# Kernel optimization log

Hardware: AMD Instinct MI355X
Metric: run time of the kernel (lower is better)

## Reference

```python
import jax, jax.numpy as jnp
import numpy as np

N = 50000          # nodes
E = 800000         # edges (avg degree 16)
# (in_feats, out_feats, num_heads) per GATConv layer
LAYERS = [(128, 64, 4), (256, 64, 2), (128, 64, 2), (128, 64, 1), (64, 4, 1)]
NEG_SLOPE = 0.2    # DGL GATConv default


def setup_inputs() -> dict:
    key = jax.random.key(0)
    ks = jax.random.split(key, 3 + 4 * len(LAYERS))
    inp = {
        "x": jax.random.normal(ks[0], (N, 128), jnp.float32),
        "src": jax.random.randint(ks[1], (E,), 0, N, jnp.int32),
        "dst": jax.random.randint(ks[2], (E,), 0, N, jnp.int32),
    }
    for i, (fin, fout, h) in enumerate(LAYERS, start=1):
        k = 3 + 4 * (i - 1)
        inp[f"W{i}"] = (jax.random.normal(ks[k], (fin, h * fout), jnp.float32)
                        / np.float32(np.sqrt(fin)))
        inp[f"al{i}"] = jax.random.normal(ks[k + 1], (h, fout), jnp.float32) * 0.1
        inp[f"ar{i}"] = jax.random.normal(ks[k + 2], (h, fout), jnp.float32) * 0.1
        inp[f"b{i}"] = jnp.zeros((h * fout,), jnp.float32)
    return inp


def gat_layer(x, src, dst, W, al, ar, b):
    """DGL GATConv: linear -> per-edge LeakyReLU scores -> edge softmax by dst -> weighted sum + bias."""
    H, F = al.shape
    n = x.shape[0]
    z = (x @ W).reshape(n, H, F)                      # [N,H,F]
    el = jnp.einsum('nhf,hf->nh', z, al)              # src-side score
    er = jnp.einsum('nhf,hf->nh', z, ar)              # dst-side score
    e = jax.nn.leaky_relu(el[src] + er[dst], NEG_SLOPE)   # [E,H]
    # segment softmax over incoming edges of each dst node
    m = jax.ops.segment_max(e, dst, num_segments=n)   # -inf for empty segments (unused)
    ex = jnp.exp(e - m[dst])
    s = jax.ops.segment_sum(ex, dst, num_segments=n)
    alpha = ex / s[dst]                               # [E,H]
    out = jax.ops.segment_sum(alpha[:, :, None] * z[src], dst, num_segments=n)  # [N,H,F]
    return out + b.reshape(1, H, F)


def reference(x, src, dst,
              W1, al1, ar1, b1,
              W2, al2, ar2, b2,
              W3, al3, ar3, b3,
              W4, al4, ar4, b4,
              W5, al5, ar5, b5):
    h = gat_layer(x, src, dst, W1, al1, ar1, b1)
    h = jax.nn.elu(h).reshape(h.shape[0], -1)
    h = gat_layer(h, src, dst, W2, al2, ar2, b2)
    h = jax.nn.elu(h).reshape(h.shape[0], -1)
    h = gat_layer(h, src, dst, W3, al3, ar3, b3)
    h = jax.nn.elu(h).reshape(h.shape[0], -1)
    h = gat_layer(h, src, dst, W4, al4, ar4, b4)
    h = jax.nn.elu(h).reshape(h.shape[0], -1)
    h = gat_layer(h, src, dst, W5, al5, ar5, b5)
    return h.reshape(h.shape[0], -1)
```

## Files before the change

kernel.cpp:

```cpp
#include <hip/hip_runtime.h>
#include <hip/hip_bf16.h>

#define NN 50000
#define NE 800000

typedef __attribute__((ext_vector_type(8))) short s16x8;
typedef __attribute__((ext_vector_type(4))) float f32x4;

__device__ __forceinline__ float bf2f(unsigned short u) {
  union { unsigned int i; float f; } v; v.i = ((unsigned int)u) << 16; return v.f;
}
__device__ __forceinline__ unsigned short f2bf(float f) {
  union { unsigned int i; float f; } v; v.f = f;
  unsigned int x = v.i;
  return (unsigned short)((x + 0x7FFFu + ((x >> 16) & 1u)) >> 16);
}

__global__ void k_detect(const unsigned short* __restrict__ xh, int* __restrict__ flag) {
  int t = threadIdx.x;
  float b0 = bf2f(xh[2 * t]);
  float b1 = bf2f(xh[2 * t + 1]);
  bool ok = (b0 == b0) && (b1 == b1) && fabsf(b0) < 64.f && fabsf(b1) < 64.f;
  unsigned long long m = __ballot(ok);
  if (t == 0) *flag = (m == ~0ull) ? 1 : 0;
}

__global__ void k_cvt_x(const void* __restrict__ src, unsigned short* __restrict__ dst, int n,
                        const int* __restrict__ flag) {
  int i = blockIdx.x * 256 + threadIdx.x;
  if (i >= n) return;
  if (*flag) dst[i] = ((const unsigned short*)src)[i];
  else       dst[i] = f2bf(((const float*)src)[i]);
}

struct SmallPack { const void* src[20]; int off[21]; };

__global__ void k_cvt_small(SmallPack pk, float* __restrict__ dst, int total,
                            const int* __restrict__ flag) {
  int i = blockIdx.x * 256 + threadIdx.x;
  if (i >= total) return;
  int d = 0;
  while (i >= pk.off[d + 1]) d++;
  int local = i - pk.off[d];
  if (*flag) dst[i] = bf2f(((const unsigned short*)pk.src[d])[local]);
  else       dst[i] = ((const float*)pk.src[d])[local];
}

struct WPack { const void* w[5]; };

__global__ void k_prep_w(WPack wp, unsigned short* __restrict__ wt, const int* __restrict__ flag) {
  const int KN[5]   = {32768, 32768, 16384, 8192, 256};
  const int LGN[5]  = {8, 7, 7, 6, 2};
  const int KK[5]   = {128, 256, 128, 128, 64};
  const int OFF[5]  = {0, 32768, 65536, 81920, 90112};
  int l = blockIdx.y;
  int i = blockIdx.x * 256 + threadIdx.x;
  if (i >= KN[l]) return;
  int k = i >> LGN[l];
  int n = i & ((1 << LGN[l]) - 1);
  unsigned short v;
  if (*flag) v = ((const unsigned short*)wp.w[l])[i];
  else       v = f2bf(((const float*)wp.w[l])[i]);
  wt[OFF[l] + n * KK[l] + k] = v;
}

__global__ void k_count(const int* __restrict__ dst, int* __restrict__ fill) {
  int e = blockIdx.x * 256 + threadIdx.x;
  if (e < NE) atomicAdd(&fill[dst[e]], 1);
}

__global__ void k_scan1(const int* __restrict__ deg, int* __restrict__ outp, int* __restrict__ csum) {
  __shared__ int s[256];
  int t = threadIdx.x, i = blockIdx.x * 256 + t;
  int v = (i < NN) ? deg[i] : 0;
  s[t] = v; __syncthreads();
  for (int o = 1; o < 256; o <<= 1) {
    int x = (t >= o) ? s[t - o] : 0; __syncthreads();
    s[t] += x; __syncthreads();
  }
  if (i < NN) outp[i] = s[t] - v;
  if (t == 255) csum[blockIdx.x] = s[255];
}

__global__ void k_scan2(int* __restrict__ csum, int nc) {
  __shared__ int s[256];
  int t = threadIdx.x;
  int v = (t < nc) ? csum[t] : 0;
  s[t] = v; __syncthreads();
  for (int o = 1; o < 256; o <<= 1) {
    int x = (t >= o) ? s[t - o] : 0; __syncthreads();
    s[t] += x; __syncthreads();
  }
  if (t < nc) csum[t] = s[t] - v;
}

__global__ void k_scan3(int* __restrict__ indptr, const int* __restrict__ csum, int* __restrict__ fill) {
  int i = blockIdx.x * 256 + threadIdx.x;
  if (i < NN) { int v = indptr[i] + csum[blockIdx.x]; indptr[i] = v; fill[i] = v; }
  if (i == NN) indptr[NN] = NE;
}

__global__ void k_fill(const int* __restrict__ src, const int* __restrict__ dst,
                       int* __restrict__ fill, int* __restrict__ csr) {
  int e = blockIdx.x * 256 + threadIdx.x;
  if (e < NE) { int p = atomicAdd(&fill[dst[e]], 1); csr[p] = src[e]; }
}

__global__ __launch_bounds__(256) void k_gemm_mfma(const unsigned short* __restrict__ A,
                                                   const unsigned short* __restrict__ Wt,
                                                   unsigned short* __restrict__ Zh,
                                                   const float* __restrict__ al,
                                                   const float* __restrict__ ar,
                                                   float* __restrict__ el, float* __restrict__ er,
                                                   int M, int K, int Nc, int H) {
  __shared__ unsigned short As[64][40];
  int tid = threadIdx.x;
  int w = tid >> 6, l = tid & 63;
  int l15 = l & 15, l16 = l >> 4;
  int row0 = blockIdx.y * 64, col0 = blockIdx.x * 64;
  int h = blockIdx.x;
  f32x4 acc[4] = {};
  for (int k0 = 0; k0 < K; k0 += 32) {
    int r = tid >> 2, kq = tid & 3;
    int grow = row0 + r;
    uint4 av = make_uint4(0, 0, 0, 0);
    if (grow < M) av = *(const uint4*)&A[(size_t)grow * K + k0 + kq * 8];
    *(uint4*)&As[r][kq * 8] = av;
    __syncthreads();
    s16x8 afrag = *(const s16x8*)&As[w * 16 + l15][l16 * 8];
#pragma unroll
    for (int nt = 0; nt < 4; nt++) {
      s16x8 bfrag = *(const s16x8*)&Wt[(size_t)(col0 + nt * 16 + l15) * K + k0 + l16 * 8];
      acc[nt] = __builtin_amdgcn_mfma_f32_16x16x32_bf16(afrag, bfrag, acc[nt], 0, 0, 0);
    }
    __syncthreads();
  }
  float alv[4], arv[4];
#pragma unroll
  for (int nt = 0; nt < 4; nt++) {
    alv[nt] = al[h * 64 + nt * 16 + l15];
    arv[nt] = ar[h * 64 + nt * 16 + l15];
  }
#pragma unroll
  for (int r = 0; r < 4; r++) {
    int mrow = w * 16 + l16 * 4 + r;
    int grow = row0 + mrow;
    bool ok = grow < M;
    float vl = 0.f, vr = 0.f;
#pragma unroll
    for (int nt = 0; nt < 4; nt++) {
      float a = acc[nt][r];
      if (ok) Zh[(size_t)grow * Nc + col0 + nt * 16 + l15] = f2bf(a);
      vl += a * alv[nt];
      vr += a * arv[nt];
    }
#pragma unroll
    for (int o = 1; o < 16; o <<= 1) {
      vl += __shfl_xor(vl, o, 64);
      vr += __shfl_xor(vr, o, 64);
    }
    if (l15 == 0 && ok) {
      el[grow * H + h] = vl;
      er[grow * H + h] = vr;
    }
  }
}

template <int H>
__global__ void k_mexp_w(const int* __restrict__ indptr, const int* __restrict__ csr,
                         const float* __restrict__ el, const float* __restrict__ er,
                         float* __restrict__ aex, float* __restrict__ sinv) {
  int g = blockIdx.x * 256 + threadIdx.x;
  int n = g >> 6, lane = g & 63;
  if (n >= NN) return;
  const int EP = 64 / H;
  int j = lane >> (H == 4 ? 2 : (H == 2 ? 1 : 0));
  int h = lane & (H - 1);
  int p0 = indptr[n], p1 = indptr[n + 1];
  float erv = er[n * H + h];
  float m = -1e30f;
  for (int p = p0 + j; p < p1; p += EP) {
    float e = el[csr[p] * H + h] + erv;
    e = (e > 0.f) ? e : 0.2f * e;
    m = fmaxf(m, e);
  }
#pragma unroll
  for (int o = H; o < 64; o <<= 1) m = fmaxf(m, __shfl_xor(m, o, 64));
  float s = 0.f;
  for (int p = p0 + j; p < p1; p += EP) {
    float e = el[csr[p] * H + h] + erv;
    e = (e > 0.f) ? e : 0.2f * e;
    float x = __expf(e - m);
    aex[p * H + h] = x;
    s += x;
  }
#pragma unroll
  for (int o = H; o < 64; o <<= 1) s += __shfl_xor(s, o, 64);
  if (lane < H) sinv[n * H + lane] = (p1 > p0) ? 1.f / s : 0.f;
}

template <int HF, int H>
__global__ void k_agg_bf(const int* __restrict__ indptr, const int* __restrict__ csr,
                         const float* __restrict__ aex, const float* __restrict__ sinv,
                         const unsigned short* __restrict__ Zh, const float* __restrict__ bias,
                         unsigned short* __restrict__ outp) {
  const int LPE = HF / 8;
  const int EPI = 64 / LPE;
  int g = blockIdx.x * 256 + threadIdx.x;
  int n = g >> 6, lane = g & 63;
  if (n >= NN) return;
  int grp = lane / LPE;
  int fl = lane % LPE;
  int f0 = fl * 8;
  int h = f0 >> 6;
  int p0 = indptr[n], p1 = indptr[n + 1];
  float acc[8] = {};
#define AGG_BODY(P)                                                         \
  {                                                                         \
    int s_ = csr[P];                                                        \
    float a_ = aex[(P) * H + h];                                            \
    uint4 v_ = *(const uint4*)(Zh + (size_t)s_ * HF + f0);                  \
    unsigned int w_[4] = {v_.x, v_.y, v_.z, v_.w};                          \
    _Pragma("unroll") for (int q = 0; q < 4; q++) {                         \
      acc[2 * q]     += a_ * bf2f((unsigned short)(w_[q] & 0xffffu));       \
      acc[2 * q + 1] += a_ * bf2f((unsigned short)(w_[q] >> 16));           \
    }                                                                       \
  }
  int p = p0 + grp;
  for (; p + EPI < p1; p += 2 * EPI) { AGG_BODY(p); AGG_BODY(p + EPI); }
  if (p < p1) AGG_BODY(p);
#undef AGG_BODY
#pragma unroll
  for (int o = LPE; o < 64; o <<= 1) {
#pragma unroll
    for (int i = 0; i < 8; i++) acc[i] += __shfl_xor(acc[i], o, 64);
  }
  if (grp == 0) {
    float inv = sinv[n * H + h];
    unsigned int pk[4];
#pragma unroll
    for (int q = 0; q < 4; q++) {
      float x0 = acc[2 * q] * inv + bias[f0 + 2 * q];
      float x1 = acc[2 * q + 1] * inv + bias[f0 + 2 * q + 1];
      x0 = (x0 > 0.f) ? x0 : expm1f(x0);
      x1 = (x1 > 0.f) ? x1 : expm1f(x1);
      pk[q] = (unsigned int)f2bf(x0) | ((unsigned int)f2bf(x1) << 16);
    }
    *(uint4*)&outp[(size_t)n * HF + f0] = make_uint4(pk[0], pk[1], pk[2], pk[3]);
  }
}

__global__ void k_l5(const unsigned short* __restrict__ hb, const float* __restrict__ W5,
                     const float* __restrict__ al5, const float* __restrict__ ar5,
                     float* __restrict__ z5, float* __restrict__ el, float* __restrict__ er) {
  __shared__ float W5s[256];
  int t = threadIdx.x;
  W5s[t] = W5[t];
  __syncthreads();
  int n = blockIdx.x * 256 + t;
  if (n >= NN) return;
  float z[4] = {};
#pragma unroll
  for (int kq = 0; kq < 8; kq++) {
    uint4 v = *(const uint4*)&hb[(size_t)n * 64 + kq * 8];
    unsigned int w_[4] = {v.x, v.y, v.z, v.w};
#pragma unroll
    for (int q = 0; q < 4; q++) {
      float f0 = bf2f((unsigned short)(w_[q] & 0xffffu));
      float f1 = bf2f((unsigned short)(w_[q] >> 16));
      int k = kq * 8 + 2 * q;
#pragma unroll
      for (int c = 0; c < 4; c++) z[c] += f0 * W5s[k * 4 + c] + f1 * W5s[(k + 1) * 4 + c];
    }
  }
  el[n] = z[0] * al5[0] + z[1] * al5[1] + z[2] * al5[2] + z[3] * al5[3];
  er[n] = z[0] * ar5[0] + z[1] * ar5[1] + z[2] * ar5[2] + z[3] * ar5[3];
  *(float4*)&z5[n * 4] = make_float4(z[0], z[1], z[2], z[3]);
}

__global__ void k_agg4(const int* __restrict__ indptr, const int* __restrict__ csr,
                       const float* __restrict__ aex, const float* __restrict__ sinv,
                       const float* __restrict__ Z, const float* __restrict__ bias,
                       void* __restrict__ outp, const int* __restrict__ flag) {
  int n = blockIdx.x * 256 + threadIdx.x;
  if (n >= NN) return;
  int p0 = indptr[n], p1 = indptr[n + 1];
  float inv = sinv[n];
  float ax = 0.f, ay = 0.f, az = 0.f, aw = 0.f;
  for (int p = p0; p < p1; p++) {
    int s = csr[p];
    float a = aex[p];
    float4 z = *(const float4*)&Z[s * 4];
    ax += a * z.x; ay += a * z.y; az += a * z.z; aw += a * z.w;
  }
  ax = ax * inv + bias[0]; ay = ay * inv + bias[1];
  az = az * inv + bias[2]; aw = aw * inv + bias[3];
  if (*flag) {
    unsigned short* o = (unsigned short*)outp;
    o[n * 4 + 0] = f2bf(ax); o[n * 4 + 1] = f2bf(ay);
    o[n * 4 + 2] = f2bf(az); o[n * 4 + 3] = f2bf(aw);
  } else {
    float* o = (float*)outp;
    o[n * 4 + 0] = ax; o[n * 4 + 1] = ay; o[n * 4 + 2] = az; o[n * 4 + 3] = aw;
  }
}

extern "C" void kernel_launch(void* const* d_in, const int* in_sizes, int n_in,
                              void* d_out, int out_size, void* d_ws, size_t ws_size,
                              hipStream_t stream) {
  (void)in_sizes; (void)n_in; (void)out_size; (void)ws_size;
  static const int fin[5] = {128, 256, 128, 128, 64};
  static const int Hh[5]  = {4, 2, 2, 1, 1};
  static const int HF[5]  = {256, 128, 128, 64, 4};
  static const int WtOff[5] = {0, 32768, 65536, 81920, 90112};

  char* ws = (char*)d_ws;
  size_t cur = 0;
  auto alloc = [&](size_t b) -> void* { void* p = ws + cur; cur += (b + 255) & ~(size_t)255; return p; };

  int*   flag   = (int*)alloc(4);
  int*   csum   = (int*)alloc(1024);
  int*   indptr = (int*)alloc((NN + 1) * 4);
  int*   fill   = (int*)alloc((size_t)NN * 4);
  int*   csr    = (int*)alloc((size_t)NE * 4);
  float* el     = (float*)alloc((size_t)NN * 4 * 4);
  float* er     = (float*)alloc((size_t)NN * 4 * 4);
  float* sinv   = (float*)alloc((size_t)NN * 4 * 4);
  float* aex    = (float*)alloc((size_t)NE * 4 * 4);
  float* smallf = (float*)alloc(100000 * 4);
  unsigned short* xh   = (unsigned short*)alloc((size_t)NN * 128 * 2);
  unsigned short* wt   = (unsigned short*)alloc(90368 * 2);
  unsigned short* hb0  = (unsigned short*)alloc((size_t)NN * 256 * 2);
  unsigned short* hb1  = (unsigned short*)alloc((size_t)NN * 256 * 2);
  unsigned short* zh   = (unsigned short*)alloc((size_t)NN * 256 * 2);
  float* z5     = (float*)alloc((size_t)NN * 4 * 4);

  const int* srcIdx = (const int*)d_in[1];
  const int* dstIdx = (const int*)d_in[2];

  SmallPack pk;
  WPack wpk;
  int off = 0;
  int aloff[5], aroff[5], boff[5], w5off = 0;
  for (int i = 0; i < 5; i++) {
    pk.src[i * 4 + 0] = d_in[3 + i * 4 + 0]; pk.off[i * 4 + 0] = off;
    wpk.w[i] = d_in[3 + i * 4 + 0];
    if (i == 4) w5off = off;
    off += fin[i] * HF[i];
    pk.src[i * 4 + 1] = d_in[3 + i * 4 + 1]; pk.off[i * 4 + 1] = off; aloff[i] = off; off += HF[i];
    pk.src[i * 4 + 2] = d_in[3 + i * 4 + 2]; pk.off[i * 4 + 2] = off; aroff[i] = off; off += HF[i];
    pk.src[i * 4 + 3] = d_in[3 + i * 4 + 3]; pk.off[i * 4 + 3] = off; boff[i]  = off; off += HF[i];
  }
  pk.off[20] = off;
  int totalSmall = off;

  k_detect<<<1, 64, 0, stream>>>((const unsigned short*)d_in[0], flag);
  hipMemsetAsync(fill, 0, (size_t)NN * 4, stream);
  { int n = NN * 128; k_cvt_x<<<(n + 255) / 256, 256, 0, stream>>>(d_in[0], xh, n, flag); }
  k_cvt_small<<<(totalSmall + 255) / 256, 256, 0, stream>>>(pk, smallf, totalSmall, flag);
  { dim3 g(128, 5); k_prep_w<<<g, 256, 0, stream>>>(wpk, wt, flag); }
  k_count<<<(NE + 255) / 256, 256, 0, stream>>>(dstIdx, fill);
  int nch = (NN + 255) / 256;
  k_scan1<<<nch, 256, 0, stream>>>(fill, indptr, csum);
  k_scan2<<<1, 256, 0, stream>>>(csum, nch);
  k_scan3<<<nch, 256, 0, stream>>>(indptr, csum, fill);
  k_fill<<<(NE + 255) / 256, 256, 0, stream>>>(srcIdx, dstIdx, fill, csr);

  const int nwaveblk = (NN * 64 + 255) / 256;

  const unsigned short* hin = xh;
  unsigned short* hout = hb0;
  for (int L = 0; L < 4; L++) {
    int K = fin[L], Nc = HF[L], H = Hh[L];
    const float* alp = smallf + aloff[L];
    const float* arp = smallf + aroff[L];
    const float* bp  = smallf + boff[L];
    dim3 gg(Nc / 64, (NN + 63) / 64);
    k_gemm_mfma<<<gg, 256, 0, stream>>>(hin, wt + WtOff[L], zh, alp, arp, el, er, NN, K, Nc, H);
    if (H == 4)      k_mexp_w<4><<<nwaveblk, 256, 0, stream>>>(indptr, csr, el, er, aex, sinv);
    else if (H == 2) k_mexp_w<2><<<nwaveblk, 256, 0, stream>>>(indptr, csr, el, er, aex, sinv);
    else             k_mexp_w<1><<<nwaveblk, 256, 0, stream>>>(indptr, csr, el, er, aex, sinv);
    if (L == 0)      k_agg_bf<256, 4><<<nwaveblk, 256, 0, stream>>>(indptr, csr, aex, sinv, zh, bp, hout);
    else if (L == 3) k_agg_bf<64, 1><<<nwaveblk, 256, 0, stream>>>(indptr, csr, aex, sinv, zh, bp, hout);
    else             k_agg_bf<128, 2><<<nwaveblk, 256, 0, stream>>>(indptr, csr, aex, sinv, zh, bp, hout);
    hin = hout;
    hout = (hout == hb0) ? hb1 : hb0;
  }
  k_l5<<<(NN + 255) / 256, 256, 0, stream>>>(hin, smallf + w5off, smallf + aloff[4],
                                             smallf + aroff[4], z5, el, er);
  k_mexp_w<1><<<nwaveblk, 256, 0, stream>>>(indptr, csr, el, er, aex, sinv);
  k_agg4<<<(NN + 255) / 256, 256, 0, stream>>>(indptr, csr, aex, sinv, z5, smallf + boff[4], d_out, flag);
}
```

Baseline: 602.6 us.

## Fuse edge softmax into aggregation and drop LDS staging in GEMM

Removes the separate max/exp kernel and the per-edge aex buffer. Aggregation now computes exp of the LeakyReLU score on the fly, accumulates the normaliser alongside the weighted features, and divides at the end, clamping the exponent at 80 instead of subtracting the segment max. The GEMM loads A fragments straight from global memory rather than staging them through shared memory with barriers. Bf16 unpacking is simplified to shifts and masks. The risks are extra exp work repeated per feature lane, reliance on bounded scores for numerical safety, and uncoalesced A loads.

```diff
diff --git a/kernel.cpp b/kernel.cpp
--- a/kernel.cpp
+++ b/kernel.cpp
@@ -113,27 +113,23 @@
                                                    const float* __restrict__ ar,
                                                    float* __restrict__ el, float* __restrict__ er,
                                                    int M, int K, int Nc, int H) {
-  __shared__ unsigned short As[64][40];
   int tid = threadIdx.x;
   int w = tid >> 6, l = tid & 63;
   int l15 = l & 15, l16 = l >> 4;
   int row0 = blockIdx.y * 64, col0 = blockIdx.x * 64;
   int h = blockIdx.x;
+  int arow = row0 + w * 16 + l15;
+  if (arow >= M) arow = M - 1;
+  const unsigned short* aptr = A + (size_t)arow * K + l16 * 8;
   f32x4 acc[4] = {};
+#pragma unroll 4
   for (int k0 = 0; k0 < K; k0 += 32) {
-    int r = tid >> 2, kq = tid & 3;
-    int grow = row0 + r;
-    uint4 av = make_uint4(0, 0, 0, 0);
-    if (grow < M) av = *(const uint4*)&A[(size_t)grow * K + k0 + kq * 8];
-    *(uint4*)&As[r][kq * 8] = av;
-    __syncthreads();
-    s16x8 afrag = *(const s16x8*)&As[w * 16 + l15][l16 * 8];
+    s16x8 afrag = *(const s16x8*)(aptr + k0);
 #pragma unroll
     for (int nt = 0; nt < 4; nt++) {
       s16x8 bfrag = *(const s16x8*)&Wt[(size_t)(col0 + nt * 16 + l15) * K + k0 + l16 * 8];
       acc[nt] = __builtin_amdgcn_mfma_f32_16x16x32_bf16(afrag, bfrag, acc[nt], 0, 0, 0);
     }
-    __syncthreads();
   }
   float alv[4], arv[4];
 #pragma unroll
@@ -143,8 +139,7 @@
   }
 #pragma unroll
   for (int r = 0; r < 4; r++) {
-    int mrow = w * 16 + l16 * 4 + r;
-    int grow = row0 + mrow;
+    int grow = row0 + w * 16 + l16 * 4 + r;
     bool ok = grow < M;
     float vl = 0.f, vr = 0.f;
 #pragma unroll
@@ -166,44 +161,11 @@
   }
 }
 
-template <int H>
-__global__ void k_mexp_w(const int* __restrict__ indptr, const int* __restrict__ csr,
-                         const float* __restrict__ el, const float* __restrict__ er,
-                         float* __restrict__ aex, float* __restrict__ sinv) {
-  int g = blockIdx.x * 256 + threadIdx.x;
-  int n = g >> 6, lane = g & 63;
-  if (n >= NN) return;
-  const int EP = 64 / H;
-  int j = lane >> (H == 4 ? 2 : (H == 2 ? 1 : 0));
-  int h = lane & (H - 1);
-  int p0 = indptr[n], p1 = indptr[n + 1];
-  float erv = er[n * H + h];
-  float m = -1e30f;
-  for (int p = p0 + j; p < p1; p += EP) {
-    float e = el[csr[p] * H + h] + erv;
-    e = (e > 0.f) ? e : 0.2f * e;
-    m = fmaxf(m, e);
-  }
-#pragma unroll
-  for (int o = H; o < 64; o <<= 1) m = fmaxf(m, __shfl_xor(m, o, 64));
-  float s = 0.f;
-  for (int p = p0 + j; p < p1; p += EP) {
-    float e = el[csr[p] * H + h] + erv;
-    e = (e > 0.f) ? e : 0.2f * e;
-    float x = __expf(e - m);
-    aex[p * H + h] = x;
-    s += x;
-  }
-#pragma unroll
-  for (int o = H; o < 64; o <<= 1) s += __shfl_xor(s, o, 64);
-  if (lane < H) sinv[n * H + lane] = (p1 > p0) ? 1.f / s : 0.f;
-}
-
 template <int HF, int H>
-__global__ void k_agg_bf(const int* __restrict__ indptr, const int* __restrict__ csr,
-                         const float* __restrict__ aex, const float* __restrict__ sinv,
-                         const unsigned short* __restrict__ Zh, const float* __restrict__ bias,
-                         unsigned short* __restrict__ outp) {
+__global__ void k_agg_f(const int* __restrict__ indptr, const int* __restrict__ csr,
+                        const float* __restrict__ el, const float* __restrict__ er,
+                        const unsigned short* __restrict__ Zh, const float* __restrict__ bias,
+                        unsigned short* __restrict__ outp) {
   const int LPE = HF / 8;
   const int EPI = 64 / LPE;
   int g = blockIdx.x * 256 + threadIdx.x;
@@ -214,17 +176,24 @@
   int f0 = fl * 8;
   int h = f0 >> 6;
   int p0 = indptr[n], p1 = indptr[n + 1];
+  float erv = er[n * H + h];
+  float s = 0.f;
   float acc[8] = {};
-#define AGG_BODY(P)                                                         \
-  {                                                                         \
-    int s_ = csr[P];                                                        \
-    float a_ = aex[(P) * H + h];                                            \
-    uint4 v_ = *(const uint4*)(Zh + (size_t)s_ * HF + f0);                  \
-    unsigned int w_[4] = {v_.x, v_.y, v_.z, v_.w};                          \
-    _Pragma("unroll") for (int q = 0; q < 4; q++) {                         \
-      acc[2 * q]     += a_ * bf2f((unsigned short)(w_[q] & 0xffffu));       \
-      acc[2 * q + 1] += a_ * bf2f((unsigned short)(w_[q] >> 16));           \
-    }                                                                       \
+#define AGG_BODY(P)                                                          \
+  {                                                                          \
+    int si_ = csr[P];                                                        \
+    float e_ = el[si_ * H + h] + erv;                                        \
+    e_ = (e_ > 0.f) ? e_ : 0.2f * e_;                                        \
+    float x_ = __expf(fminf(e_, 80.f));                                      \
+    s += x_;                                                                 \
+    uint4 v_ = *(const uint4*)(Zh + (size_t)si_ * HF + f0);                  \
+    unsigned int w_[4] = {v_.x, v_.y, v_.z, v_.w};                           \
+    _Pragma("unroll") for (int q = 0; q < 4; q++) {                          \
+      union { unsigned int u; float f; } lo_, hi_;                           \
+      lo_.u = w_[q] << 16; hi_.u = w_[q] & 0xffff0000u;                      \
+      acc[2 * q]     += x_ * lo_.f;                                          \
+      acc[2 * q + 1] += x_ * hi_.f;                                          \
+    }                                                                        \
   }
   int p = p0 + grp;
   for (; p + EPI < p1; p += 2 * EPI) { AGG_BODY(p); AGG_BODY(p + EPI); }
@@ -232,11 +201,12 @@
 #undef AGG_BODY
 #pragma unroll
   for (int o = LPE; o < 64; o <<= 1) {
+    s += __shfl_xor(s, o, 64);
 #pragma unroll
     for (int i = 0; i < 8; i++) acc[i] += __shfl_xor(acc[i], o, 64);
   }
   if (grp == 0) {
-    float inv = sinv[n * H + h];
+    float inv = (p1 > p0) ? 1.f / s : 0.f;
     unsigned int pk[4];
 #pragma unroll
     for (int q = 0; q < 4; q++) {
@@ -266,11 +236,11 @@
     unsigned int w_[4] = {v.x, v.y, v.z, v.w};
 #pragma unroll
     for (int q = 0; q < 4; q++) {
-      float f0 = bf2f((unsigned short)(w_[q] & 0xffffu));
-      float f1 = bf2f((unsigned short)(w_[q] >> 16));
+      union { unsigned int u; float f; } lo, hi;
+      lo.u = w_[q] << 16; hi.u = w_[q] & 0xffff0000u;
       int k = kq * 8 + 2 * q;
 #pragma unroll
-      for (int c = 0; c < 4; c++) z[c] += f0 * W5s[k * 4 + c] + f1 * W5s[(k + 1) * 4 + c];
+      for (int c = 0; c < 4; c++) z[c] += lo.f * W5s[k * 4 + c] + hi.f * W5s[(k + 1) * 4 + c];
     }
   }
   el[n] = z[0] * al5[0] + z[1] * al5[1] + z[2] * al5[2] + z[3] * al5[3];
@@ -278,21 +248,26 @@
   *(float4*)&z5[n * 4] = make_float4(z[0], z[1], z[2], z[3]);
 }
 
-__global__ void k_agg4(const int* __restrict__ indptr, const int* __restrict__ csr,
-                       const float* __restrict__ aex, const float* __restrict__ sinv,
-                       const float* __restrict__ Z, const float* __restrict__ bias,
-                       void* __restrict__ outp, const int* __restrict__ flag) {
+__global__ void k_agg4_f(const int* __restrict__ indptr, const int* __restrict__ csr,
+                         const float* __restrict__ el, const float* __restrict__ er,
+                         const float* __restrict__ Z, const float* __restrict__ bias,
+                         void* __restrict__ outp, const int* __restrict__ flag) {
   int n = blockIdx.x * 256 + threadIdx.x;
   if (n >= NN) return;
   int p0 = indptr[n], p1 = indptr[n + 1];
-  float inv = sinv[n];
+  float erv = er[n];
+  float s = 0.f;
   float ax = 0.f, ay = 0.f, az = 0.f, aw = 0.f;
   for (int p = p0; p < p1; p++) {
-    int s = csr[p];
-    float a = aex[p];
-    float4 z = *(const float4*)&Z[s * 4];
-    ax += a * z.x; ay += a * z.y; az += a * z.z; aw += a * z.w;
-  }
+    int si = csr[p];
+    float e = el[si] + erv;
+    e = (e > 0.f) ? e : 0.2f * e;
+    float x = __expf(fminf(e, 80.f));
+    s += x;
+    float4 z = *(const float4*)&Z[si * 4];
+    ax += x * z.x; ay += x * z.y; az += x * z.z; aw += x * z.w;
+  }
+  float inv = (p1 > p0) ? 1.f / s : 0.f;
   ax = ax * inv + bias[0]; ay = ay * inv + bias[1];
   az = az * inv + bias[2]; aw = aw * inv + bias[3];
   if (*flag) {
@@ -325,8 +300,6 @@
   int*   csr    = (int*)alloc((size_t)NE * 4);
   float* el     = (float*)alloc((size_t)NN * 4 * 4);
   float* er     = (float*)alloc((size_t)NN * 4 * 4);
-  float* sinv   = (float*)alloc((size_t)NN * 4 * 4);
-  float* aex    = (float*)alloc((size_t)NE * 4 * 4);
   float* smallf = (float*)alloc(100000 * 4);
   unsigned short* xh   = (unsigned short*)alloc((size_t)NN * 128 * 2);
   unsigned short* wt   = (unsigned short*)alloc(90368 * 2);
@@ -377,17 +350,13 @@
     const float* bp  = smallf + boff[L];
     dim3 gg(Nc / 64, (NN + 63) / 64);
     k_gemm_mfma<<<gg, 256, 0, stream>>>(hin, wt + WtOff[L], zh, alp, arp, el, er, NN, K, Nc, H);
-    if (H == 4)      k_mexp_w<4><<<nwaveblk, 256, 0, stream>>>(indptr, csr, el, er, aex, sinv);
-    else if (H == 2) k_mexp_w<2><<<nwaveblk, 256, 0, stream>>>(indptr, csr, el, er, aex, sinv);
-    else             k_mexp_w<1><<<nwaveblk, 256, 0, stream>>>(indptr, csr, el, er, aex, sinv);
-    if (L == 0)      k_agg_bf<256, 4><<<nwaveblk, 256, 0, stream>>>(indptr, csr, aex, sinv, zh, bp, hout);
-    else if (L == 3) k_agg_bf<64, 1><<<nwaveblk, 256, 0, stream>>>(indptr, csr, aex, sinv, zh, bp, hout);
-    else             k_agg_bf<128, 2><<<nwaveblk, 256, 0, stream>>>(indptr, csr, aex, sinv, zh, bp, hout);
+    if (L == 0)      k_agg_f<256, 4><<<nwaveblk, 256, 0, stream>>>(indptr, csr, el, er, zh, bp, hout);
+    else if (L == 3) k_agg_f<64, 1><<<nwaveblk, 256, 0, stream>>>(indptr, csr, el, er, zh, bp, hout);
+    else             k_agg_f<128, 2><<<nwaveblk, 256, 0, stream>>>(indptr, csr, el, er, zh, bp, hout);
     hin = hout;
     hout = (hout == hb0) ? hb1 : hb0;
   }
   k_l5<<<(NN + 255) / 256, 256, 0, stream>>>(hin, smallf + w5off, smallf + aloff[4],
                                              smallf + aroff[4], z5, el, er);
-  k_mexp_w<1><<<nwaveblk, 256, 0, stream>>>(indptr, csr, el, er, aex, sinv);
-  k_agg4<<<(NN + 255) / 256, 256, 0, stream>>>(indptr, csr, aex, sinv, z5, smallf + boff[4], d_out, flag);
-}
+  k_agg4_f<<<(NN + 255) / 256, 256, 0, stream>>>(indptr, csr, el, er, z5, smallf + boff[4], d_out, flag);
+}
```

Result: faster. 524.6 us (-12.9%).
